# Kernel optimization log

Measured on AMD Instinct MI355X. Metric: run time of the kernel, lower is better.

The kernel has to match this reference:

```python
import jax, jax.numpy as jnp
import numpy as np

B, K, N, C, H, D_CA = 64, 75, 2025, 256, 8, 2
HID = 4 * C


def _ln(x, w, b):
    m = x.mean(-1, keepdims=True)
    v = ((x - m) ** 2).mean(-1, keepdims=True)
    return (x - m) / jnp.sqrt(v + 1e-5) * w + b


def setup_inputs() -> dict:
    key = jax.random.key(0)
    ks = jax.random.split(key, 8)
    def w(k, shape):
        return jax.random.normal(k, shape, jnp.float32) * 0.02
    return {
        "x_cls": jax.random.normal(ks[0], (B, K, C), jnp.float32),
        "x_patch": jax.random.normal(ks[1], (B, N, C), jnp.float32),
        "ln1_w": jnp.ones((D_CA, C), jnp.float32),
        "ln1_b": jnp.zeros((D_CA, C), jnp.float32),
        "q_w": w(ks[2], (D_CA, C, C)),
        "k_w": w(ks[3], (D_CA, C, C)),
        "v_w": w(ks[4], (D_CA, C, C)),
        "proj_w": w(ks[5], (D_CA, C, C)),
        "proj_b": jnp.zeros((D_CA, C), jnp.float32),
        "ln2_w": jnp.ones((D_CA, C), jnp.float32),
        "ln2_b": jnp.zeros((D_CA, C), jnp.float32),
        "fc1_w": w(ks[6], (D_CA, HID, C)),
        "fc1_b": jnp.zeros((D_CA, HID), jnp.float32),
        "fc2_w": w(ks[7], (D_CA, C, HID)),
        "fc2_b": jnp.zeros((D_CA, C), jnp.float32),
        "gamma1": jnp.full((D_CA, C), 1e-4, jnp.float32),
        "gamma2": jnp.full((D_CA, C), 1e-4, jnp.float32),
    }


def reference(x_cls, x_patch, ln1_w, ln1_b, q_w, k_w, v_w, proj_w, proj_b,
              ln2_w, ln2_b, fc1_w, fc1_b, fc2_w, fc2_b, gamma1, gamma2):
    hd = C // H
    scale = hd ** -0.5
    for i in range(D_CA):  # fixed depth_CA=2 class-attention blocks
        u = jnp.concatenate([x_cls, x_patch], axis=1)          # (B, K+N, C)
        un = _ln(u, ln1_w[i], ln1_b[i])
        # Class_Attention: queries only from first K tokens, keys/values from all
        q = (un[:, :K] @ q_w[i].T).reshape(B, K, H, hd) * scale
        kk = (un @ k_w[i].T).reshape(B, K + N, H, hd)
        vv = (un @ v_w[i].T).reshape(B, K + N, H, hd)
        attn = jax.nn.softmax(jnp.einsum('bkhd,bnhd->bhkn', q, kk), axis=-1)
        o = jnp.einsum('bhkn,bnhd->bkhd', attn, vv).reshape(B, K, C)
        x_cls = x_cls + gamma1[i] * (o @ proj_w[i].T + proj_b[i])
        # MLP block on class tokens only
        xn = _ln(x_cls, ln2_w[i], ln2_b[i])
        h = jax.nn.gelu(xn @ fc1_w[i].T + fc1_b[i], approximate=False)
        x_cls = x_cls + gamma2[i] * (h @ fc2_w[i].T + fc2_b[i])
    return x_cls
```

## Files before the change

### kernel.cpp

```cpp
#include <hip/hip_runtime.h>
#include <cstdint>
#include <cstddef>

typedef unsigned short u16;
typedef float f32x4 __attribute__((ext_vector_type(4)));
typedef short s16x8 __attribute__((ext_vector_type(8)));
typedef unsigned short u16x4 __attribute__((ext_vector_type(4)));
typedef __bf16 bf16x8 __attribute__((ext_vector_type(8)));

#define DEV static __device__ __forceinline__

DEV u16 f2bf(float f) {
  uint32_t x = __float_as_uint(f);
  return (u16)((x + 0x7fffu + ((x >> 16) & 1u)) >> 16);
}

DEV f32x4 mfma16(bf16x8 a, bf16x8 b, f32x4 c) {
  return __builtin_amdgcn_mfma_f32_16x16x32_bf16(a, b, c, 0, 0, 0);
}

DEV void mfma_bf16_asm(f32x4& acc, s16x8 a, s16x8 b) {
  asm volatile("v_mfma_f32_16x16x32_bf16 %0, %1, %2, %0" : "+v"(acc) : "v"(a), "v"(b));
}

DEV uint32_t pkbf(float lo, float hi) {
  uint32_t r;
  asm("v_cvt_pk_bf16_f32 %0, %1, %2" : "=v"(r) : "v"(lo), "v"(hi));
  return r;
}

__global__ __launch_bounds__(256) void k_prep(
    const float* __restrict__ x_cls, const float* __restrict__ x_patch,
    const float* __restrict__ k_w, const float* __restrict__ v_w,
    const float* __restrict__ q_w, const float* __restrict__ proj_w,
    const float* __restrict__ fc1_w, const float* __restrict__ fc2_w,
    const float* __restrict__ ln1_w, const float* __restrict__ ln1_b,
    const float* __restrict__ ln2_w, const float* __restrict__ ln2_b,
    const float* __restrict__ fc1_b,
    u16* __restrict__ kvp, u16* __restrict__ qp, u16* __restrict__ pjp,
    u16* __restrict__ f1p, u16* __restrict__ f2p,
    float* __restrict__ bias_kv, float* __restrict__ bias_q, float* __restrict__ bias_f1,
    float* __restrict__ xc, u16* __restrict__ nxp) {
  const int jb = blockIdx.x;
  const int lane = threadIdx.x & 63;
  if (jb >= 2736) {
    int wv = (jb - 2736) * 4 + (threadIdx.x >> 6);
    if (wv >= 129600) return;
    float4 v = ((const float4*)(x_patch + (size_t)wv * 256))[lane];
    float s = v.x + v.y + v.z + v.w;
    float q = v.x * v.x + v.y * v.y + v.z * v.z + v.w * v.w;
#pragma unroll
    for (int m = 1; m < 64; m <<= 1) {
      s += __shfl_xor(s, m, 64);
      q += __shfl_xor(q, m, 64);
    }
    float mean = s * (1.f / 256.f);
    float var = q * (1.f / 256.f) - mean * mean;
    float rstd = rsqrtf(var + 1e-5f);
    u16x4 o;
    o[0] = f2bf((v.x - mean) * rstd);
    o[1] = f2bf((v.y - mean) * rstd);
    o[2] = f2bf((v.z - mean) * rstd);
    o[3] = f2bf((v.w - mean) * rstd);
    ((u16x4*)(nxp + (size_t)wv * 256))[lane] = o;
    return;
  }
  if (jb >= 1536) {
    int i = (jb - 1536) * 256 + threadIdx.x;
    ((float4*)xc)[i] = ((const float4*)x_cls)[i];
    return;
  }
  const int layer = jb >= 768 ? 1 : 0;
  const int j = jb - layer * 768;
  const float* W;
  const float* lw = ln1_w + layer * 256;
  const float* lb = ln1_b + layer * 256;
  const float* b0 = nullptr;
  u16* Wout;
  float* bout = nullptr;
  int rowoff;
  if (j < 64)       { W = k_w + layer * 65536;    Wout = kvp + layer * 131072;         bout = bias_kv + layer * 512;       rowoff = j * 4; }
  else if (j < 128) { W = v_w + layer * 65536;    Wout = kvp + layer * 131072 + 65536; bout = bias_kv + layer * 512 + 256; rowoff = (j - 64) * 4; }
  else if (j < 192) { W = q_w + layer * 65536;    Wout = qp + layer * 65536;           bout = bias_q + layer * 256;        rowoff = (j - 128) * 4; }
  else if (j < 448) { W = fc1_w + layer * 262144; lw = ln2_w + layer * 256; lb = ln2_b + layer * 256; b0 = fc1_b + layer * 1024;
                      Wout = f1p + layer * 262144; bout = bias_f1 + layer * 1024;      rowoff = (j - 192) * 4; }
  else if (j < 512) { W = proj_w + layer * 65536; lw = nullptr;                        Wout = pjp + layer * 65536;         rowoff = (j - 448) * 4; }
  else              { W = fc2_w + layer * 262144; lw = nullptr;                        Wout = f2p + layer * 262144;        rowoff = (j - 512) * 4; }
  const int wv = rowoff + (threadIdx.x >> 6);
  float4 w4 = ((const float4*)(W + (size_t)wv * 256))[lane];
  u16x4 o;
  if (lw) {
    float4 s4 = ((const float4*)lw)[lane];
    o[0] = f2bf(w4.x * s4.x); o[1] = f2bf(w4.y * s4.y);
    o[2] = f2bf(w4.z * s4.z); o[3] = f2bf(w4.w * s4.w);
  } else {
    o[0] = f2bf(w4.x); o[1] = f2bf(w4.y); o[2] = f2bf(w4.z); o[3] = f2bf(w4.w);
  }
  ((u16x4*)(Wout + (size_t)wv * 256))[lane] = o;
  if (bout) {
    float4 t4 = ((const float4*)lb)[lane];
    float d = w4.x * t4.x + w4.y * t4.y + w4.z * t4.z + w4.w * t4.w;
#pragma unroll
    for (int m = 1; m < 64; m <<= 1) d += __shfl_xor(d, m, 64);
    if (lane == 0) bout[wv] = (b0 ? b0[wv] : 0.f) + d;
  }
}

__global__ __launch_bounds__(256) void k_norm(const float* __restrict__ src,
                                              u16* __restrict__ out, int ntok) {
  int wv = blockIdx.x * 4 + (threadIdx.x >> 6), lane = threadIdx.x & 63;
  if (wv >= ntok) return;
  float4 v = ((const float4*)(src + (size_t)wv * 256))[lane];
  float s = v.x + v.y + v.z + v.w;
  float q = v.x * v.x + v.y * v.y + v.z * v.z + v.w * v.w;
#pragma unroll
  for (int m = 1; m < 64; m <<= 1) {
    s += __shfl_xor(s, m, 64);
    q += __shfl_xor(q, m, 64);
  }
  float mean = s * (1.f / 256.f);
  float var = q * (1.f / 256.f) - mean * mean;
  float rstd = rsqrtf(var + 1e-5f);
  u16x4 o;
  o[0] = f2bf((v.x - mean) * rstd);
  o[1] = f2bf((v.y - mean) * rstd);
  o[2] = f2bf((v.z - mean) * rstd);
  o[3] = f2bf((v.w - mean) * rstd);
  ((u16x4*)(out + (size_t)wv * 256))[lane] = o;
}

__global__ __launch_bounds__(256) void k_gemm6(const u16* __restrict__ A,
                                               const u16* __restrict__ Bw,
                                               int N, int K, int mode,
                                               int lognby, float scale,
                                               const float* __restrict__ bias,
                                               const float* __restrict__ gamma,
                                               u16* __restrict__ obf,
                                               float* __restrict__ of32) {
  __shared__ __align__(16) char smA[8192];
  __shared__ __align__(16) char smB[16384];
  const int tid = threadIdx.x, lane = tid & 63, wid = tid >> 6;
  const int wm = wid >> 1, wn = wid & 1;
  const int bid = blockIdx.x;
  const int by = bid & ((1 << lognby) - 1), bx = bid >> lognby;
  const int m0 = bx * 64, n0 = by * 128;
  const int g = lane >> 4, l15 = lane & 15;

  f32x4 acc[2][4] = {};

  for (int k0 = 0; k0 < K; k0 += 64) {
#pragma unroll
    for (int c = 0; c < 2; c++) {
      int ee = tid + 256 * c;
      int row = ee >> 3, sl = ee & 7;
      s16x8 av = *(const s16x8*)(A + (size_t)(m0 + row) * K + k0 + sl * 8);
      *(s16x8*)(smA + row * 128 + ((sl * 16) ^ ((row & 7) << 4))) = av;
    }
#pragma unroll
    for (int c = 0; c < 4; c++) {
      int ee = tid + 256 * c;
      int row = ee >> 3, sl = ee & 7;
      s16x8 bv = *(const s16x8*)(Bw + (size_t)(n0 + row) * K + k0 + sl * 8);
      *(s16x8*)(smB + row * 128 + ((sl * 16) ^ ((row & 7) << 4))) = bv;
    }
    __syncthreads();
    s16x8 af[2][2], bfr[4][2];
#pragma unroll
    for (int s = 0; s < 2; s++) {
#pragma unroll
      for (int i = 0; i < 2; i++) {
        int r = wm * 32 + i * 16 + l15;
        af[i][s] = *(const s16x8*)(smA + r * 128 + (((s * 4 + g) * 16) ^ ((r & 7) << 4)));
      }
#pragma unroll
      for (int jj = 0; jj < 4; jj++) {
        int n = wn * 64 + jj * 16 + l15;
        bfr[jj][s] = *(const s16x8*)(smB + n * 128 + (((s * 4 + g) * 16) ^ ((n & 7) << 4)));
      }
    }
#pragma unroll
    for (int s = 0; s < 2; s++)
#pragma unroll
      for (int i = 0; i < 2; i++)
#pragma unroll
        for (int jj = 0; jj < 4; jj++)
          mfma_bf16_asm(acc[i][jj], af[i][s], bfr[jj][s]);
    __syncthreads();
  }
  asm volatile("s_nop 7\n\ts_nop 7" ::: "memory");

#pragma unroll
  for (int i = 0; i < 2; i++) {
#pragma unroll
    for (int jj = 0; jj < 4; jj++) {
      int gmBase = m0 + wm * 32 + i * 16 + g * 4;
      int gn = n0 + wn * 64 + jj * 16 + l15;
      float bs = bias[gn];
#pragma unroll
      for (int r = 0; r < 4; r++) {
        int gm = gmBase + r;
        float v = acc[i][jj][r] + bs;
        if (mode == 1) {
          obf[(size_t)gm * N + gn] = f2bf(v * scale);
        } else if (mode == 2) {
          of32[(size_t)gm * N + gn] += gamma[gn] * v;
        } else {
          obf[(size_t)gm * N + gn] = f2bf(0.5f * v * (1.f + erff(v * 0.70710678118654752f)));
        }
      }
    }
  }
}

__global__ __launch_bounds__(256, 2) void k_fattn(const u16* __restrict__ qb,
                                                  const u16* __restrict__ uncls,
                                                  const u16* __restrict__ nxp,
                                                  const u16* __restrict__ wkv,
                                                  const float* __restrict__ bias_kv,
                                                  float* __restrict__ pO,
                                                  float* __restrict__ pml) {
  __shared__ __align__(16) char arena[50176];
  __shared__ float mlS[4][80];
  const int bid = blockIdx.x;
  const int b = bid & 63, h = (bid >> 6) & 7, half = bid >> 9;
  const int tid = threadIdx.x, lane = tid & 63, w = tid >> 6;
  const int l15 = lane & 15, g = lane >> 4;
  const int tbase = half * 33, tend = tbase + 33;

  u16* WL = (u16*)arena;
  char* wb = arena + 32768 + w * 4352;
  uint32_t* KL = (uint32_t*)wb;
  uint32_t* PB = (uint32_t*)wb;
  u16* VL = (u16*)(wb + 2048);

  for (int it = tid; it < 2048; it += 256) {
    int row = it >> 5, c16 = it & 31;
    int srcRow = (row < 32) ? (h * 32 + row) : (256 + h * 32 + (row - 32));
    s16x8 w8 = *(const s16x8*)(wkv + (size_t)srcRow * 256 + c16 * 8);
    *(s16x8*)(WL + row * 256 + (((c16 * 16) ^ ((row & 7) << 4)) >> 1)) = w8;
  }

  float bk[2][4], bvb[2][4];
#pragma unroll
  for (int s2 = 0; s2 < 2; s2++)
#pragma unroll
    for (int r = 0; r < 4; r++) {
      bk[s2][r] = bias_kv[h * 32 + s2 * 16 + 4 * g + r];
      bvb[s2][r] = bias_kv[256 + h * 32 + s2 * 16 + 4 * g + r];
    }

  bf16x8 bq[5];
#pragma unroll
  for (int qt = 0; qt < 5; qt++) {
    int q = qt * 16 + l15; if (q > 74) q = 74;
    s16x8 qv = *(const s16x8*)(qb + (size_t)(b * 75 + q) * 256 + h * 32 + g * 8);
    bq[qt] = __builtin_bit_cast(bf16x8, qv);
  }

  f32x4 acc[5][2] = {};
  float llc[5];
#pragma unroll
  for (int qt = 0; qt < 5; qt++) llc[qt] = 0.f;

  __syncthreads();

  const int xw = (l15 & 7) << 4;
  const int xk = (l15 & 3) << 2;

  for (int tt = tbase + w; tt < tend; tt += 4) {
    const int t0 = tt * 32;
    int tA = t0 + l15;      if (tA > 2099) tA = 2099;
    int tB = t0 + 16 + l15; if (tB > 2099) tB = 2099;
    const u16* rowA = (tA < 75) ? uncls + ((size_t)b * 75 + tA) * 256
                                : nxp + ((size_t)b * 2025 + (tA - 75)) * 256;
    const u16* rowB = (tB < 75) ? uncls + ((size_t)b * 75 + tB) * 256
                                : nxp + ((size_t)b * 2025 + (tB - 75)) * 256;

    f32x4 aK[2][2] = {}, aV[2][2] = {};
    __builtin_amdgcn_s_setprio(1);
#pragma unroll
    for (int ks = 0; ks < 8; ks++) {
      bf16x8 nA = __builtin_bit_cast(bf16x8, *(const s16x8*)(rowA + ks * 32 + g * 8));
      bf16x8 nB = __builtin_bit_cast(bf16x8, *(const s16x8*)(rowB + ks * 32 + g * 8));
      const int cb = (ks * 64 + g * 16) ^ xw;
      bf16x8 k0 = __builtin_bit_cast(bf16x8, *(const s16x8*)(WL + l15 * 256 + (cb >> 1)));
      bf16x8 k1 = __builtin_bit_cast(bf16x8, *(const s16x8*)(WL + (16 + l15) * 256 + (cb >> 1)));
      bf16x8 w0 = __builtin_bit_cast(bf16x8, *(const s16x8*)(WL + (32 + l15) * 256 + (cb >> 1)));
      bf16x8 w1 = __builtin_bit_cast(bf16x8, *(const s16x8*)(WL + (48 + l15) * 256 + (cb >> 1)));
      aK[0][0] = mfma16(k0, nA, aK[0][0]);
      aK[0][1] = mfma16(k0, nB, aK[0][1]);
      aK[1][0] = mfma16(k1, nA, aK[1][0]);
      aK[1][1] = mfma16(k1, nB, aK[1][1]);
      aV[0][0] = mfma16(w0, nA, aV[0][0]);
      aV[0][1] = mfma16(w0, nB, aV[0][1]);
      aV[1][0] = mfma16(w1, nA, aV[1][0]);
      aV[1][1] = mfma16(w1, nB, aV[1][1]);
    }
    __builtin_amdgcn_s_setprio(0);

#pragma unroll
    for (int s2 = 0; s2 < 2; s2++)
#pragma unroll
      for (int u = 0; u < 2; u++) {
        const int trow = u * 16 + l15;
        f32x4 kk4 = aK[s2][u];
        uint2 pk2;
        pk2.x = pkbf(kk4[0] + bk[s2][0], kk4[1] + bk[s2][1]);
        pk2.y = pkbf(kk4[2] + bk[s2][2], kk4[3] + bk[s2][3]);
        *(uint2*)&KL[trow * 16 + ((s2 * 8 + 2 * g) ^ ((trow & 3) << 2))] = pk2;
        f32x4 vv4 = aV[s2][u];
        uint32_t pv0 = pkbf(vv4[0] + bvb[s2][0], vv4[1] + bvb[s2][1]);
        uint32_t pv1 = pkbf(vv4[2] + bvb[s2][2], vv4[3] + bvb[s2][3]);
        *(uint32_t*)&VL[trow * 36 + s2 * 16 + 4 * g] = pv0;
        *(uint32_t*)&VL[trow * 36 + s2 * 16 + 4 * g + 2] = pv1;
      }

    uint4 ka = *(const uint4*)&KL[l15 * 16 + ((4 * g) ^ xk)];
    uint4 kb = *(const uint4*)&KL[(16 + l15) * 16 + ((4 * g) ^ xk)];
    bf16x8 bA = __builtin_bit_cast(bf16x8, ka);
    bf16x8 bB = __builtin_bit_cast(bf16x8, kb);
    s16x8 v0, v1;
#pragma unroll
    for (int e = 0; e < 8; e++) {
      v0[e] = (short)VL[(8 * g + e) * 36 + l15];
      v1[e] = (short)VL[(8 * g + e) * 36 + 16 + l15];
    }
    bf16x8 bv0 = __builtin_bit_cast(bf16x8, v0);
    bf16x8 bv1 = __builtin_bit_cast(bf16x8, v1);

    const bool lastTile = (t0 == 2080);

#pragma unroll
    for (int qt = 0; qt < 5; qt++) {
      f32x4 z = {0.f, 0.f, 0.f, 0.f};
      f32x4 sA = mfma16(bA, bq[qt], z);
      f32x4 sB = mfma16(bB, bq[qt], z);
      if (lastTile && g >= 1) {
        sB[0] = sB[1] = sB[2] = sB[3] = -1e30f;
      }
      f32x4 pA, pB;
#pragma unroll
      for (int r = 0; r < 4; r++) {
        pA[r] = exp2f(sA[r]);
        pB[r] = exp2f(sB[r]);
      }
      llc[qt] += pA[0] + pA[1] + pA[2] + pA[3] + pB[0] + pB[1] + pB[2] + pB[3];
      uint32_t* Pu = &PB[l15 * 20];
      Pu[2 * g]     = pkbf(pA[0], pA[1]);
      Pu[2 * g + 1] = pkbf(pA[2], pA[3]);
      Pu[8 + 2 * g]     = pkbf(pB[0], pB[1]);
      Pu[8 + 2 * g + 1] = pkbf(pB[2], pB[3]);
      uint4 pu = *(const uint4*)&PB[l15 * 20 + 4 * g];
      bf16x8 bp = __builtin_bit_cast(bf16x8, pu);
      acc[qt][0] = mfma16(bp, bv0, acc[qt][0]);
      acc[qt][1] = mfma16(bp, bv1, acc[qt][1]);
    }
  }

#pragma unroll
  for (int qt = 0; qt < 5; qt++) {
    float t = llc[qt];
    t += __shfl_xor(t, 16, 64);
    t += __shfl_xor(t, 32, 64);
    llc[qt] = t;
  }
  __syncthreads();
  float* MC = (float*)arena;
#pragma unroll
  for (int qt = 0; qt < 5; qt++)
#pragma unroll
    for (int dh = 0; dh < 2; dh++)
#pragma unroll
      for (int r = 0; r < 4; r++) {
        int q = qt * 16 + 4 * g + r;
        MC[w * 2560 + q * 32 + dh * 16 + l15] = acc[qt][dh][r];
      }
  if (lane < 16) {
#pragma unroll
    for (int qt = 0; qt < 5; qt++) mlS[w][qt * 16 + l15] = llc[qt];
  }
  __syncthreads();

  if (tid < 75) {
    float L = mlS[0][tid] + mlS[1][tid] + mlS[2][tid] + mlS[3][tid];
    pml[(size_t)bid * 80 + tid] = L;
  }
  for (int idx = tid; idx < 2400; idx += 256) {
    int q = idx >> 5;
    float O = MC[q * 32 + (idx & 31)] + MC[2560 + q * 32 + (idx & 31)] +
              MC[5120 + q * 32 + (idx & 31)] + MC[7680 + q * 32 + (idx & 31)];
    pO[(size_t)bid * 2400 + idx] = O;
  }
}

__global__ __launch_bounds__(256) void k_acomb(const float* __restrict__ pO,
                                               const float* __restrict__ pml,
                                               u16* __restrict__ obf) {
  const int bid = blockIdx.x;
  const int b = bid & 63, h = bid >> 6;
  const int tid = threadIdx.x;
  for (int idx = tid; idx < 2400; idx += 256) {
    int q = idx >> 5, d = idx & 31;
    float L = pml[(size_t)bid * 80 + q] + pml[(size_t)(bid + 512) * 80 + q];
    float O = pO[(size_t)bid * 2400 + idx] + pO[(size_t)(bid + 512) * 2400 + idx];
    obf[(size_t)(b * 75 + q) * 256 + h * 32 + d] = f2bf(O / L);
  }
}

extern "C" void kernel_launch(void* const* d_in, const int* in_sizes, int n_in,
                              void* d_out, int out_size, void* d_ws, size_t ws_size,
                              hipStream_t stream) {
  const float* x_cls   = (const float*)d_in[0];
  const float* x_patch = (const float*)d_in[1];
  const float* ln1_w   = (const float*)d_in[2];
  const float* ln1_b   = (const float*)d_in[3];
  const float* q_w     = (const float*)d_in[4];
  const float* k_w     = (const float*)d_in[5];
  const float* v_w     = (const float*)d_in[6];
  const float* proj_w  = (const float*)d_in[7];
  const float* proj_b  = (const float*)d_in[8];
  const float* ln2_w   = (const float*)d_in[9];
  const float* ln2_b   = (const float*)d_in[10];
  const float* fc1_w   = (const float*)d_in[11];
  const float* fc1_b   = (const float*)d_in[12];
  const float* fc2_w   = (const float*)d_in[13];
  const float* fc2_b   = (const float*)d_in[14];
  const float* gamma1  = (const float*)d_in[15];
  const float* gamma2  = (const float*)d_in[16];
  float* xc = (float*)d_out;

  char* ws = (char*)d_ws;
  size_t off = 0;
  auto alloc = [&](size_t bytes) {
    char* p = ws + off;
    off += (bytes + 255) & ~(size_t)255;
    return p;
  };
  u16* nxp   = (u16*)alloc(129600ull * 256 * 2);
  u16* uncls = (u16*)alloc(4800ull * 256 * 2);
  u16* qb    = (u16*)alloc(4800ull * 256 * 2);
  u16* ob    = (u16*)alloc(4800ull * 256 * 2);
  u16* xn    = (u16*)alloc(4800ull * 256 * 2);
  u16* hb    = (u16*)alloc(4800ull * 1024 * 2);
  u16* qp    = (u16*)alloc(2ull * 65536 * 2);
  u16* kvp   = (u16*)alloc(2ull * 131072 * 2);
  u16* pjp   = (u16*)alloc(2ull * 65536 * 2);
  u16* f1p   = (u16*)alloc(2ull * 262144 * 2);
  u16* f2p   = (u16*)alloc(2ull * 262144 * 2);
  float* bias_kv = (float*)alloc(2ull * 512 * 4);
  float* bias_q  = (float*)alloc(2ull * 256 * 4);
  float* bias_f1 = (float*)alloc(2ull * 1024 * 4);
  float* pO  = (float*)alloc(1024ull * 2400 * 4);
  float* pml = (float*)alloc(1024ull * 80 * 4);

  k_prep<<<35136, 256, 0, stream>>>(x_cls, x_patch, k_w, v_w, q_w, proj_w, fc1_w, fc2_w,
                                    ln1_w, ln1_b, ln2_w, ln2_b, fc1_b,
                                    kvp, qp, pjp, f1p, f2p,
                                    bias_kv, bias_q, bias_f1, xc, nxp);

  const float qscale = 0.25503489f;
  for (int i = 0; i < 2; i++) {
    k_norm<<<1200, 256, 0, stream>>>(xc, uncls, 4800);
    k_gemm6<<<150, 256, 0, stream>>>(uncls, qp + i * 65536, 256, 256, 1, 1, qscale,
                                     bias_q + i * 256, nullptr, qb, nullptr);
    k_fattn<<<1024, 256, 0, stream>>>(qb, uncls, nxp, kvp + i * 131072,
                                      bias_kv + i * 512, pO, pml);
    k_acomb<<<512, 256, 0, stream>>>(pO, pml, ob);
    k_gemm6<<<150, 256, 0, stream>>>(ob, pjp + i * 65536, 256, 256, 2, 1, 0.f,
                                     proj_b + i * 256, gamma1 + i * 256, nullptr, xc);
    k_norm<<<1200, 256, 0, stream>>>(xc, xn, 4800);
    k_gemm6<<<600, 256, 0, stream>>>(xn, f1p + i * 262144, 1024, 256, 3, 3, 0.f,
                                     bias_f1 + i * 1024, nullptr, hb, nullptr);
    k_gemm6<<<150, 256, 0, stream>>>(hb, f2p + i * 262144, 256, 1024, 2, 1, 0.f,
                                     fc2_b + i * 256, gamma2 + i * 256, nullptr, xc);
  }
}
```

Measured before the change: 337.3 us.

## Permute Q head-dim layout so K and P feed MFMA directly from registers

The Q projection epilogue now writes each head's 32 dims in a permuted slot order, so the K-projection accumulators and the softmax probabilities can be packed straight into MFMA operands without a round trip through LDS. Because the contraction order is permuted consistently on both sides, the per-tile LDS staging for K and P is removed and only V is still staged (with a matching row permutation). The smaller LDS footprint lets launch bounds ask for 3 blocks per CU instead of 2, which may raise register pressure or cause spills.

```diff
diff --git a/kernel.cpp b/kernel.cpp
--- a/kernel.cpp
+++ b/kernel.cpp
@@ -201,7 +201,9 @@
         int gm = gmBase + r;
         float v = acc[i][jj][r] + bs;
         if (mode == 1) {
-          obf[(size_t)gm * N + gn] = f2bf(v * scale);
+          int hd = gn & 31;
+          int slot = 8 * ((hd & 15) >> 2) + 4 * (hd >> 4) + (hd & 3);
+          obf[(size_t)gm * N + (gn & ~31) + slot] = f2bf(v * scale);
         } else if (mode == 2) {
           of32[(size_t)gm * N + gn] += gamma[gn] * v;
         } else {
@@ -212,14 +214,14 @@
   }
 }
 
-__global__ __launch_bounds__(256, 2) void k_fattn(const u16* __restrict__ qb,
+__global__ __launch_bounds__(256, 3) void k_fattn(const u16* __restrict__ qb,
                                                   const u16* __restrict__ uncls,
                                                   const u16* __restrict__ nxp,
                                                   const u16* __restrict__ wkv,
                                                   const float* __restrict__ bias_kv,
                                                   float* __restrict__ pO,
                                                   float* __restrict__ pml) {
-  __shared__ __align__(16) char arena[50176];
+  __shared__ __align__(16) char arena[41984];
   __shared__ float mlS[4][80];
   const int bid = blockIdx.x;
   const int b = bid & 63, h = (bid >> 6) & 7, half = bid >> 9;
@@ -228,10 +230,7 @@
   const int tbase = half * 33, tend = tbase + 33;
 
   u16* WL = (u16*)arena;
-  char* wb = arena + 32768 + w * 4352;
-  uint32_t* KL = (uint32_t*)wb;
-  uint32_t* PB = (uint32_t*)wb;
-  u16* VL = (u16*)(wb + 2048);
+  u16* VL = (u16*)(arena + 32768 + w * 2304);
 
   for (int it = tid; it < 2048; it += 256) {
     int row = it >> 5, c16 = it & 31;
@@ -265,7 +264,7 @@
   __syncthreads();
 
   const int xw = (l15 & 7) << 4;
-  const int xk = (l15 & 3) << 2;
+  const int srowA = 8 * (l15 >> 2) + (l15 & 3);
 
   for (int tt = tbase + w; tt < tend; tt += 4) {
     const int t0 = tt * 32;
@@ -298,27 +297,29 @@
     }
     __builtin_amdgcn_s_setprio(0);
 
-#pragma unroll
-    for (int s2 = 0; s2 < 2; s2++)
-#pragma unroll
-      for (int u = 0; u < 2; u++) {
-        const int trow = u * 16 + l15;
-        f32x4 kk4 = aK[s2][u];
-        uint2 pk2;
-        pk2.x = pkbf(kk4[0] + bk[s2][0], kk4[1] + bk[s2][1]);
-        pk2.y = pkbf(kk4[2] + bk[s2][2], kk4[3] + bk[s2][3]);
-        *(uint2*)&KL[trow * 16 + ((s2 * 8 + 2 * g) ^ ((trow & 3) << 2))] = pk2;
-        f32x4 vv4 = aV[s2][u];
-        uint32_t pv0 = pkbf(vv4[0] + bvb[s2][0], vv4[1] + bvb[s2][1]);
-        uint32_t pv1 = pkbf(vv4[2] + bvb[s2][2], vv4[3] + bvb[s2][3]);
-        *(uint32_t*)&VL[trow * 36 + s2 * 16 + 4 * g] = pv0;
-        *(uint32_t*)&VL[trow * 36 + s2 * 16 + 4 * g + 2] = pv1;
-      }
-
-    uint4 ka = *(const uint4*)&KL[l15 * 16 + ((4 * g) ^ xk)];
-    uint4 kb = *(const uint4*)&KL[(16 + l15) * 16 + ((4 * g) ^ xk)];
-    bf16x8 bA = __builtin_bit_cast(bf16x8, ka);
-    bf16x8 bB = __builtin_bit_cast(bf16x8, kb);
+    uint4 kwA, kwB;
+    kwA.x = pkbf(aK[0][0][0] + bk[0][0], aK[0][0][1] + bk[0][1]);
+    kwA.y = pkbf(aK[0][0][2] + bk[0][2], aK[0][0][3] + bk[0][3]);
+    kwA.z = pkbf(aK[1][0][0] + bk[1][0], aK[1][0][1] + bk[1][1]);
+    kwA.w = pkbf(aK[1][0][2] + bk[1][2], aK[1][0][3] + bk[1][3]);
+    kwB.x = pkbf(aK[0][1][0] + bk[0][0], aK[0][1][1] + bk[0][1]);
+    kwB.y = pkbf(aK[0][1][2] + bk[0][2], aK[0][1][3] + bk[0][3]);
+    kwB.z = pkbf(aK[1][1][0] + bk[1][0], aK[1][1][1] + bk[1][1]);
+    kwB.w = pkbf(aK[1][1][2] + bk[1][2], aK[1][1][3] + bk[1][3]);
+    bf16x8 bA = __builtin_bit_cast(bf16x8, kwA);
+    bf16x8 bB = __builtin_bit_cast(bf16x8, kwB);
+
+#pragma unroll
+    for (int s2 = 0; s2 < 2; s2++) {
+      uint2 pv0, pv1;
+      pv0.x = pkbf(aV[s2][0][0] + bvb[s2][0], aV[s2][0][1] + bvb[s2][1]);
+      pv0.y = pkbf(aV[s2][0][2] + bvb[s2][2], aV[s2][0][3] + bvb[s2][3]);
+      pv1.x = pkbf(aV[s2][1][0] + bvb[s2][0], aV[s2][1][1] + bvb[s2][1]);
+      pv1.y = pkbf(aV[s2][1][2] + bvb[s2][2], aV[s2][1][3] + bvb[s2][3]);
+      *(uint2*)&VL[srowA * 36 + s2 * 16 + 4 * g] = pv0;
+      *(uint2*)&VL[(srowA + 4) * 36 + s2 * 16 + 4 * g] = pv1;
+    }
+
     s16x8 v0, v1;
 #pragma unroll
     for (int e = 0; e < 8; e++) {
@@ -345,13 +346,12 @@
         pB[r] = exp2f(sB[r]);
       }
       llc[qt] += pA[0] + pA[1] + pA[2] + pA[3] + pB[0] + pB[1] + pB[2] + pB[3];
-      uint32_t* Pu = &PB[l15 * 20];
-      Pu[2 * g]     = pkbf(pA[0], pA[1]);
-      Pu[2 * g + 1] = pkbf(pA[2], pA[3]);
-      Pu[8 + 2 * g]     = pkbf(pB[0], pB[1]);
-      Pu[8 + 2 * g + 1] = pkbf(pB[2], pB[3]);
-      uint4 pu = *(const uint4*)&PB[l15 * 20 + 4 * g];
-      bf16x8 bp = __builtin_bit_cast(bf16x8, pu);
+      uint4 pw;
+      pw.x = pkbf(pA[0], pA[1]);
+      pw.y = pkbf(pA[2], pA[3]);
+      pw.z = pkbf(pB[0], pB[1]);
+      pw.w = pkbf(pB[2], pB[3]);
+      bf16x8 bp = __builtin_bit_cast(bf16x8, pw);
       acc[qt][0] = mfma16(bp, bv0, acc[qt][0]);
       acc[qt][1] = mfma16(bp, bv1, acc[qt][1]);
     }
```

Result: slower. 357.8 us (+6.1%).

## Process two token tiles per wave iteration to reuse LDS weight fragments

Applied to the files above, without the earlier changes.

Each wave now handles pairs of 32-token tiles. The K/V projection weight fragments are loaded from LDS once per k-step and shared by the MFMAs of both tiles, which halves LDS weight reads and exposes more independent MFMA work. The attention part is moved into a lambda that runs once per tile, and the V store is merged into a single 64-bit write. The cost is doubled accumulator registers, which may raise register pressure against the 2-blocks-per-CU launch bound, plus a branch for the odd final tile.

```diff
diff --git a/kernel.cpp b/kernel.cpp
--- a/kernel.cpp
+++ b/kernel.cpp
@@ -225,7 +225,7 @@
   const int b = bid & 63, h = (bid >> 6) & 7, half = bid >> 9;
   const int tid = threadIdx.x, lane = tid & 63, w = tid >> 6;
   const int l15 = lane & 15, g = lane >> 4;
-  const int tbase = half * 33, tend = tbase + 33;
+  const int tbase = half * 33;
 
   u16* WL = (u16*)arena;
   char* wb = arena + 32768 + w * 4352;
@@ -267,37 +267,7 @@
   const int xw = (l15 & 7) << 4;
   const int xk = (l15 & 3) << 2;
 
-  for (int tt = tbase + w; tt < tend; tt += 4) {
-    const int t0 = tt * 32;
-    int tA = t0 + l15;      if (tA > 2099) tA = 2099;
-    int tB = t0 + 16 + l15; if (tB > 2099) tB = 2099;
-    const u16* rowA = (tA < 75) ? uncls + ((size_t)b * 75 + tA) * 256
-                                : nxp + ((size_t)b * 2025 + (tA - 75)) * 256;
-    const u16* rowB = (tB < 75) ? uncls + ((size_t)b * 75 + tB) * 256
-                                : nxp + ((size_t)b * 2025 + (tB - 75)) * 256;
-
-    f32x4 aK[2][2] = {}, aV[2][2] = {};
-    __builtin_amdgcn_s_setprio(1);
-#pragma unroll
-    for (int ks = 0; ks < 8; ks++) {
-      bf16x8 nA = __builtin_bit_cast(bf16x8, *(const s16x8*)(rowA + ks * 32 + g * 8));
-      bf16x8 nB = __builtin_bit_cast(bf16x8, *(const s16x8*)(rowB + ks * 32 + g * 8));
-      const int cb = (ks * 64 + g * 16) ^ xw;
-      bf16x8 k0 = __builtin_bit_cast(bf16x8, *(const s16x8*)(WL + l15 * 256 + (cb >> 1)));
-      bf16x8 k1 = __builtin_bit_cast(bf16x8, *(const s16x8*)(WL + (16 + l15) * 256 + (cb >> 1)));
-      bf16x8 w0 = __builtin_bit_cast(bf16x8, *(const s16x8*)(WL + (32 + l15) * 256 + (cb >> 1)));
-      bf16x8 w1 = __builtin_bit_cast(bf16x8, *(const s16x8*)(WL + (48 + l15) * 256 + (cb >> 1)));
-      aK[0][0] = mfma16(k0, nA, aK[0][0]);
-      aK[0][1] = mfma16(k0, nB, aK[0][1]);
-      aK[1][0] = mfma16(k1, nA, aK[1][0]);
-      aK[1][1] = mfma16(k1, nB, aK[1][1]);
-      aV[0][0] = mfma16(w0, nA, aV[0][0]);
-      aV[0][1] = mfma16(w0, nB, aV[0][1]);
-      aV[1][0] = mfma16(w1, nA, aV[1][0]);
-      aV[1][1] = mfma16(w1, nB, aV[1][1]);
-    }
-    __builtin_amdgcn_s_setprio(0);
-
+  auto attend = [&](f32x4 (&aK)[2][2], f32x4 (&aV)[2][2], int t0) {
 #pragma unroll
     for (int s2 = 0; s2 < 2; s2++)
 #pragma unroll
@@ -309,10 +279,10 @@
         pk2.y = pkbf(kk4[2] + bk[s2][2], kk4[3] + bk[s2][3]);
         *(uint2*)&KL[trow * 16 + ((s2 * 8 + 2 * g) ^ ((trow & 3) << 2))] = pk2;
         f32x4 vv4 = aV[s2][u];
-        uint32_t pv0 = pkbf(vv4[0] + bvb[s2][0], vv4[1] + bvb[s2][1]);
-        uint32_t pv1 = pkbf(vv4[2] + bvb[s2][2], vv4[3] + bvb[s2][3]);
-        *(uint32_t*)&VL[trow * 36 + s2 * 16 + 4 * g] = pv0;
-        *(uint32_t*)&VL[trow * 36 + s2 * 16 + 4 * g + 2] = pv1;
+        uint2 pv2;
+        pv2.x = pkbf(vv4[0] + bvb[s2][0], vv4[1] + bvb[s2][1]);
+        pv2.y = pkbf(vv4[2] + bvb[s2][2], vv4[3] + bvb[s2][3]);
+        *(uint2*)&VL[trow * 36 + s2 * 16 + 4 * g] = pv2;
       }
 
     uint4 ka = *(const uint4*)&KL[l15 * 16 + ((4 * g) ^ xk)];
@@ -355,6 +325,62 @@
       acc[qt][0] = mfma16(bp, bv0, acc[qt][0]);
       acc[qt][1] = mfma16(bp, bv1, acc[qt][1]);
     }
+  };
+
+  for (int p = w; p < 17; p += 4) {
+    const int t0a = (tbase + 2 * p) * 32;
+    const bool has2 = (2 * p + 1) < 33;
+    const int t0b = t0a + 32;
+
+    int tA0 = t0a + l15;      if (tA0 > 2099) tA0 = 2099;
+    int tB0 = t0a + 16 + l15; if (tB0 > 2099) tB0 = 2099;
+    int tA1 = t0b + l15;      if (tA1 > 2099) tA1 = 2099;
+    int tB1 = t0b + 16 + l15; if (tB1 > 2099) tB1 = 2099;
+    const u16* rowA0 = (tA0 < 75) ? uncls + ((size_t)b * 75 + tA0) * 256
+                                  : nxp + ((size_t)b * 2025 + (tA0 - 75)) * 256;
+    const u16* rowB0 = (tB0 < 75) ? uncls + ((size_t)b * 75 + tB0) * 256
+                                  : nxp + ((size_t)b * 2025 + (tB0 - 75)) * 256;
+    const u16* rowA1 = (tA1 < 75) ? uncls + ((size_t)b * 75 + tA1) * 256
+                                  : nxp + ((size_t)b * 2025 + (tA1 - 75)) * 256;
+    const u16* rowB1 = (tB1 < 75) ? uncls + ((size_t)b * 75 + tB1) * 256
+                                  : nxp + ((size_t)b * 2025 + (tB1 - 75)) * 256;
+
+    f32x4 aK0[2][2] = {}, aV0[2][2] = {}, aK1[2][2] = {}, aV1[2][2] = {};
+    __builtin_amdgcn_s_setprio(1);
+#pragma unroll
+    for (int ks = 0; ks < 8; ks++) {
+      const int cb = (ks * 64 + g * 16) ^ xw;
+      bf16x8 k0 = __builtin_bit_cast(bf16x8, *(const s16x8*)(WL + l15 * 256 + (cb >> 1)));
+      bf16x8 k1 = __builtin_bit_cast(bf16x8, *(const s16x8*)(WL + (16 + l15) * 256 + (cb >> 1)));
+      bf16x8 w0 = __builtin_bit_cast(bf16x8, *(const s16x8*)(WL + (32 + l15) * 256 + (cb >> 1)));
+      bf16x8 w1 = __builtin_bit_cast(bf16x8, *(const s16x8*)(WL + (48 + l15) * 256 + (cb >> 1)));
+      bf16x8 nA0 = __builtin_bit_cast(bf16x8, *(const s16x8*)(rowA0 + ks * 32 + g * 8));
+      bf16x8 nB0 = __builtin_bit_cast(bf16x8, *(const s16x8*)(rowB0 + ks * 32 + g * 8));
+      aK0[0][0] = mfma16(k0, nA0, aK0[0][0]);
+      aK0[0][1] = mfma16(k0, nB0, aK0[0][1]);
+      aK0[1][0] = mfma16(k1, nA0, aK0[1][0]);
+      aK0[1][1] = mfma16(k1, nB0, aK0[1][1]);
+      aV0[0][0] = mfma16(w0, nA0, aV0[0][0]);
+      aV0[0][1] = mfma16(w0, nB0, aV0[0][1]);
+      aV0[1][0] = mfma16(w1, nA0, aV0[1][0]);
+      aV0[1][1] = mfma16(w1, nB0, aV0[1][1]);
+      if (has2) {
+        bf16x8 nA1 = __builtin_bit_cast(bf16x8, *(const s16x8*)(rowA1 + ks * 32 + g * 8));
+        bf16x8 nB1 = __builtin_bit_cast(bf16x8, *(const s16x8*)(rowB1 + ks * 32 + g * 8));
+        aK1[0][0] = mfma16(k0, nA1, aK1[0][0]);
+        aK1[0][1] = mfma16(k0, nB1, aK1[0][1]);
+        aK1[1][0] = mfma16(k1, nA1, aK1[1][0]);
+        aK1[1][1] = mfma16(k1, nB1, aK1[1][1]);
+        aV1[0][0] = mfma16(w0, nA1, aV1[0][0]);
+        aV1[0][1] = mfma16(w0, nB1, aV1[0][1]);
+        aV1[1][0] = mfma16(w1, nA1, aV1[1][0]);
+        aV1[1][1] = mfma16(w1, nB1, aV1[1][1]);
+      }
+    }
+    __builtin_amdgcn_s_setprio(0);
+
+    attend(aK0, aV0, t0a);
+    if (has2) attend(aK1, aV1, t0b);
   }
 
 #pragma unroll
```

Result: slower. 360.0 us (+6.7%).
